# Performance work log

Hardware: AMD Instinct MI355X
Metric: run time of the kernel (lower is better)

## Reference

```python
import jax, jax.numpy as jnp
import numpy as np

N, IN_F, OUT_F, EMB = 8192, 256, 128, 16

def setup_inputs() -> dict:
    key = jax.random.key(0)
    ks = jax.random.split(key, 6)
    s_in, s_out = 1.0 / np.sqrt(IN_F), 1.0 / np.sqrt(OUT_F)
    return {
        "h": jax.random.normal(ks[0], (N, IN_F), jnp.float32),
        "eps": jax.random.normal(ks[1], (N, OUT_F), jnp.float32),
        "a_str": jax.random.uniform(ks[2], (N, N), jnp.float32),  # precomputed exp_adj kernel (positive)
        "W_fc": jax.random.normal(ks[3], (IN_F, OUT_F), jnp.float32) * s_in,
        "W_k": jax.random.normal(ks[4], (OUT_F, EMB), jnp.float32) * s_out,
        "W_q": jax.random.normal(ks[5], (OUT_F, EMB), jnp.float32) * s_out,
    }

def reference(h, eps, a_str, W_fc, W_k, W_q):
    # h0 = fc(h); h <- N(0,1) sample (eps) + h0
    hh = eps + h @ W_fc                      # [N, OUT_F]
    k = hh @ W_k                             # [N, EMB]
    q = hh @ W_q                             # [N, EMB]
    a_att = jax.nn.softmax(k @ q.T, axis=-1) # [N, N]
    a = a_str * a_att                        # elementwise structural mask
    a = a / jnp.sum(a, axis=-1, keepdims=True)  # renormalize rows
    return a @ hh                            # [N, OUT_F]
```

## Files before the change

### kernel.cpp

```cpp
#include <hip/hip_runtime.h>
#include <hip/hip_bf16.h>

#define NN     8192
#define INF_   256
#define OF     128
#define EMBD   16
#define QB     16
#define JB     128
#define NST    (NN / JB)
#define JSPLIT 4
#define NSTP   (NST / JSPLIT)

typedef __attribute__((ext_vector_type(4))) float f32x4;
typedef __attribute__((ext_vector_type(8))) short s16x8;

__device__ __forceinline__ unsigned short f2bf(float x) {
  unsigned u = __builtin_bit_cast(unsigned, x);
  return (unsigned short)((u + 0x7FFFu + ((u >> 16) & 1u)) >> 16);
}

__device__ __forceinline__ float fexp2(float x) {
#if __has_builtin(__builtin_amdgcn_exp2f)
  return __builtin_amdgcn_exp2f(x);
#else
  return exp2f(x);
#endif
}

__global__ __launch_bounds__(256) void k_hh(const float* __restrict__ h,
                                            const float* __restrict__ eps,
                                            const float* __restrict__ Wfc,
                                            float* __restrict__ hh) {
  const int tx = threadIdx.x & 31;
  const int ty = threadIdx.x >> 5;
  const int i0 = blockIdx.x * 16 + ty * 2;
  const int c  = tx * 4;
  f32x4 a0 = *(const f32x4*)&eps[(size_t)i0 * OF + c];
  f32x4 a1 = *(const f32x4*)&eps[(size_t)(i0 + 1) * OF + c];
  const float* h0 = h + (size_t)i0 * INF_;
  const float* h1 = h0 + INF_;
#pragma unroll 2
  for (int kk = 0; kk < INF_; kk += 4) {
    const f32x4 ha = *(const f32x4*)&h0[kk];
    const f32x4 hb = *(const f32x4*)&h1[kk];
#pragma unroll
    for (int u = 0; u < 4; ++u) {
      const f32x4 wv = *(const f32x4*)&Wfc[(size_t)(kk + u) * OF + c];
      a0 += ha[u] * wv;
      a1 += hb[u] * wv;
    }
  }
  *(f32x4*)&hh[(size_t)i0 * OF + c]       = a0;
  *(f32x4*)&hh[(size_t)(i0 + 1) * OF + c] = a1;
}

__global__ __launch_bounds__(256) void k_kq(const float* __restrict__ hh,
                                            const float* __restrict__ Wk,
                                            const float* __restrict__ Wq,
                                            float* __restrict__ kp,
                                            float* __restrict__ qp) {
  const int t   = blockIdx.x * 256 + threadIdx.x;
  const int i   = t >> 3;
  const int sub = t & 7;
  const float* W = (sub < 4) ? Wk : Wq;
  const int e    = (sub & 3) * 4;
  const float* hr = hh + (size_t)i * OF;
  f32x4 acc = {0.f, 0.f, 0.f, 0.f};
#pragma unroll 4
  for (int o = 0; o < OF; o += 4) {
    const f32x4 hv = *(const f32x4*)&hr[o];
#pragma unroll
    for (int u = 0; u < 4; ++u) {
      const f32x4 wv = *(const f32x4*)&W[(size_t)(o + u) * EMBD + e];
      acc += hv[u] * wv;
    }
  }
  if (sub < 4) {
    acc *= 1.4426950408889634f;
    *(f32x4*)&kp[(size_t)i * EMBD + e] = acc;
  } else {
    *(f32x4*)&qp[(size_t)i * EMBD + e] = acc;
  }
}

__global__ __launch_bounds__(256) void k_tr(const float* __restrict__ hh,
                                            short* __restrict__ hhT) {
  __shared__ float tile[64][65];
  const int i0 = blockIdx.x * 64;
  const int o0 = blockIdx.y * 64;
  const int c = threadIdx.x & 63;
  const int r = threadIdx.x >> 6;
#pragma unroll
  for (int rr = 0; rr < 16; ++rr) {
    const int ii = rr * 4 + r;
    tile[ii][c] = hh[(size_t)(i0 + ii) * OF + o0 + c];
  }
  __syncthreads();
#pragma unroll
  for (int rr = 0; rr < 16; ++rr) {
    const int oo = rr * 4 + r;
    hhT[(size_t)(o0 + oo) * NN + i0 + c] = (short)f2bf(tile[c][oo]);
  }
}

__global__ __launch_bounds__(256) void k_attn(const float* __restrict__ Astr,
                                              const float* __restrict__ kp,
                                              const float* __restrict__ qp,
                                              const short* __restrict__ hhT,
                                              float* __restrict__ accP,
                                              float* __restrict__ dP) {
  __shared__ __align__(16) float qbuf[2][JB * EMBD];
  __shared__ __align__(16) short wbuf[2][QB * JB];

  const int tid = threadIdx.x;
  const int l   = tid & 63;
  const int row = tid >> 4;
  const int g   = tid & 15;
  const int ctp = tid >> 6;
  const int h4  = l >> 4;
  const int ln  = l & 15;
  const int rb  = blockIdx.x * QB;
  const int p   = blockIdx.y;
  const int t0  = p * NSTP;
  const int jr  = tid >> 1;
  const int eh  = (tid & 1) * 2;

  float kreg[16];
  {
    const f32x4* kv = (const f32x4*)(kp + (size_t)(rb + row) * EMBD);
#pragma unroll
    for (int i = 0; i < 4; ++i) {
      f32x4 v = kv[i];
      kreg[i * 4 + 0] = v.x; kreg[i * 4 + 1] = v.y;
      kreg[i * 4 + 2] = v.z; kreg[i * 4 + 3] = v.w;
    }
  }
  f32x4 acc0 = {0.f, 0.f, 0.f, 0.f};
  f32x4 acc1 = {0.f, 0.f, 0.f, 0.f};
  float dpart = 0.f;

  const size_t arow = (size_t)(rb + row) * NN;
  const int swzw = row & 7;
  const int qsw0 = (jr >> 3) & 7;

  {
    const float* src = qp + (size_t)(t0 * JB + jr) * EMBD + eh * 4;
    f32x4 v0 = *(const f32x4*)src;
    f32x4 v1 = *(const f32x4*)(src + 4);
    *(f32x4*)&qbuf[0][((jr * 4 + eh)     ^ qsw0) * 4] = v0;
    *(f32x4*)&qbuf[0][((jr * 4 + eh + 1) ^ qsw0) * 4] = v1;
  }
  f32x4 aA[2], aB[2];
  aA[0] = *(const f32x4*)(Astr + arow + t0 * JB + g * 8);
  aA[1] = *(const f32x4*)(Astr + arow + t0 * JB + g * 8 + 4);
  __syncthreads();

  auto STEP = [&](int t, f32x4 (&acur)[2], f32x4 (&anxt)[2], int par) {
    const int jb = t * JB;
    const int tn = (t + 1 < t0 + NSTP) ? (t + 1) : t0;
    const int jn = tn * JB;
    const float* qsrc = qp + (size_t)(jn + jr) * EMBD + eh * 4;
    f32x4 qv0 = *(const f32x4*)qsrc;
    f32x4 qv1 = *(const f32x4*)(qsrc + 4);
    s16x8 bfr[2][4];
#pragma unroll
    for (int cc = 0; cc < 2; ++cc) {
      const size_t bbase = (size_t)(ctp * 32 + cc * 16 + ln) * NN + jb + h4 * 8;
#pragma unroll
      for (int kt = 0; kt < 4; ++kt)
        bfr[cc][kt] = *(const s16x8*)(hhT + bbase + kt * 32);
    }
    anxt[0] = *(const f32x4*)(Astr + arow + jn + g * 8);
    anxt[1] = *(const f32x4*)(Astr + arow + jn + g * 8 + 4);
    float s[8];
#pragma unroll
    for (int jj = 0; jj < 8; ++jj) {
      const int j  = g * 8 + jj;
      const int sw = (j >> 3) & 7;
      const f32x4 q0 = *(const f32x4*)&qbuf[par][((j * 4 + 0) ^ sw) * 4];
      const f32x4 q1 = *(const f32x4*)&qbuf[par][((j * 4 + 1) ^ sw) * 4];
      const f32x4 q2 = *(const f32x4*)&qbuf[par][((j * 4 + 2) ^ sw) * 4];
      const f32x4 q3 = *(const f32x4*)&qbuf[par][((j * 4 + 3) ^ sw) * 4];
      float u0 = kreg[0] * q0.x, u1 = kreg[1] * q0.y;
      u0 = fmaf(kreg[2],  q0.z, u0); u1 = fmaf(kreg[3],  q0.w, u1);
      u0 = fmaf(kreg[4],  q1.x, u0); u1 = fmaf(kreg[5],  q1.y, u1);
      u0 = fmaf(kreg[6],  q1.z, u0); u1 = fmaf(kreg[7],  q1.w, u1);
      u0 = fmaf(kreg[8],  q2.x, u0); u1 = fmaf(kreg[9],  q2.y, u1);
      u0 = fmaf(kreg[10], q2.z, u0); u1 = fmaf(kreg[11], q2.w, u1);
      u0 = fmaf(kreg[12], q3.x, u0); u1 = fmaf(kreg[13], q3.y, u1);
      u0 = fmaf(kreg[14], q3.z, u0); u1 = fmaf(kreg[15], q3.w, u1);
      s[jj] = u0 + u1;
    }
    s16x8 wpack;
    {
      const float* ac = (const float*)&acur[0];
#pragma unroll
      for (int jj = 0; jj < 8; ++jj) {
        const float wv = ac[jj] * fexp2(fminf(s[jj] - 32.0f, 80.0f));
        dpart += wv;
        wpack[jj] = (short)f2bf(wv);
      }
    }
    *(s16x8*)&wbuf[par][row * JB + ((g ^ swzw) * 8)] = wpack;
    *(f32x4*)&qbuf[par ^ 1][((jr * 4 + eh)     ^ qsw0) * 4] = qv0;
    *(f32x4*)&qbuf[par ^ 1][((jr * 4 + eh + 1) ^ qsw0) * 4] = qv1;
    __syncthreads();
    s16x8 afr[4];
#pragma unroll
    for (int kt = 0; kt < 4; ++kt)
      afr[kt] = *(const s16x8*)&wbuf[par][ln * JB + (((kt * 4 + h4) ^ (ln & 7)) * 8)];
#pragma unroll
    for (int kt = 0; kt < 4; ++kt) {
      acc0 = __builtin_amdgcn_mfma_f32_16x16x32_bf16(afr[kt], bfr[0][kt], acc0, 0, 0, 0);
      acc1 = __builtin_amdgcn_mfma_f32_16x16x32_bf16(afr[kt], bfr[1][kt], acc1, 0, 0, 0);
    }
  };

  for (int t = t0; t < t0 + NSTP; t += 2) {
    STEP(t,     aA, aB, 0);
    STEP(t + 1, aB, aA, 1);
  }

  float d = dpart;
  d += __shfl_xor(d, 1, 16);
  d += __shfl_xor(d, 2, 16);
  d += __shfl_xor(d, 4, 16);
  d += __shfl_xor(d, 8, 16);
  if (g == 0) dP[(size_t)p * NN + rb + row] = d;
#pragma unroll
  for (int r = 0; r < 4; ++r) {
    const int lrow = h4 * 4 + r;
    float* orow = accP + ((size_t)p * NN + rb + lrow) * OF + ctp * 32 + ln;
    orow[0]  = acc0[r];
    orow[16] = acc1[r];
  }
}

__global__ __launch_bounds__(256) void k_comb(const float* __restrict__ accP,
                                              const float* __restrict__ dP,
                                              float* __restrict__ out) {
  const int idx = blockIdx.x * 256 + threadIdx.x;
  const int row = idx >> 5;
  const int cq  = (idx & 31) * 4;
  float D = 0.f;
  f32x4 s = {0.f, 0.f, 0.f, 0.f};
#pragma unroll
  for (int pp = 0; pp < JSPLIT; ++pp) {
    D += dP[(size_t)pp * NN + row];
    s += *(const f32x4*)&accP[((size_t)pp * NN + row) * OF + cq];
  }
  const float inv = 1.0f / D;
  f32x4 r = s * inv;
  *(f32x4*)&out[(size_t)row * OF + cq] = r;
}

extern "C" void kernel_launch(void* const* d_in, const int* in_sizes, int n_in,
                              void* d_out, int out_size, void* d_ws, size_t ws_size,
                              hipStream_t stream) {
  const float* h   = (const float*)d_in[0];
  const float* eps = (const float*)d_in[1];
  const float* As  = (const float*)d_in[2];
  const float* Wfc = (const float*)d_in[3];
  const float* Wk  = (const float*)d_in[4];
  const float* Wq  = (const float*)d_in[5];
  float* out = (float*)d_out;

  char* ws = (char*)d_ws;
  float* kp   = (float*)(ws);
  float* qp   = (float*)(ws + (512u << 10));
  short* hhT  = (short*)(ws + (1u << 20));
  float* accP = (float*)(ws + (3u << 20));
  float* hh   = (float*)(ws + (3u << 20));
  float* dP   = (float*)(ws + (19u << 20));

  k_hh<<<NN / 16, 256, 0, stream>>>(h, eps, Wfc, hh);
  k_kq<<<(NN * 8) / 256, 256, 0, stream>>>(hh, Wk, Wq, kp, qp);
  k_tr<<<dim3(NN / 64, OF / 64), 256, 0, stream>>>(hh, hhT);
  k_attn<<<dim3(NN / QB, JSPLIT), 256, 0, stream>>>(As, kp, qp, hhT, accP, dP);
  k_comb<<<(NN * OF / 4) / 256, 256, 0, stream>>>(accP, dP, out);
}
```

Before: 500.3 us.

## Compute attention scores with split-bf16 MFMA and per-wave 32-row tiles

The score computation k·q, previously done with scalar FMAs over q staged in shared memory, now runs on 32x32x16 bf16 MFMAs using a hi/lo bf16 split of k and q (three MFMAs) to keep near-fp32 accuracy. Each wave independently handles 32 query rows over an 8-way j-split, with no shared memory or block barriers, and feeds the bf16 weights straight into register MFMA operands via a row permutation. This removes LDS traffic and syncs and the VALU-bound score math. In exchange it uses more registers and more accP partial storage (8 splits), and drops the exponent clamp.

```diff
diff --git a/kernel.cpp b/kernel.cpp
--- a/kernel.cpp
+++ b/kernel.cpp
@@ -5,20 +5,24 @@
 #define INF_   256
 #define OF     128
 #define EMBD   16
-#define QB     16
-#define JB     128
-#define NST    (NN / JB)
-#define JSPLIT 4
-#define NSTP   (NST / JSPLIT)
-
-typedef __attribute__((ext_vector_type(4))) float f32x4;
-typedef __attribute__((ext_vector_type(8))) short s16x8;
+#define JSPLIT 8
+#define JCH    (NN / JSPLIT)
+#define KV     32
+#define NSTEP  (JCH / KV)
+
+typedef __attribute__((ext_vector_type(4)))  float          f32x4;
+typedef __attribute__((ext_vector_type(16))) float          f32x16;
+typedef __attribute__((ext_vector_type(8)))  short          s16x8;
+typedef __attribute__((ext_vector_type(4)))  unsigned int   u32x4;
+typedef __attribute__((ext_vector_type(4)))  unsigned short u16x4;
 
 __device__ __forceinline__ unsigned short f2bf(float x) {
   unsigned u = __builtin_bit_cast(unsigned, x);
   return (unsigned short)((u + 0x7FFFu + ((u >> 16) & 1u)) >> 16);
 }
-
+__device__ __forceinline__ float bf2f(unsigned short h) {
+  return __builtin_bit_cast(float, (unsigned)h << 16);
+}
 __device__ __forceinline__ float fexp2(float x) {
 #if __has_builtin(__builtin_amdgcn_exp2f)
   return __builtin_amdgcn_exp2f(x);
@@ -57,8 +61,10 @@
 __global__ __launch_bounds__(256) void k_kq(const float* __restrict__ hh,
                                             const float* __restrict__ Wk,
                                             const float* __restrict__ Wq,
-                                            float* __restrict__ kp,
-                                            float* __restrict__ qp) {
+                                            unsigned short* __restrict__ kph,
+                                            unsigned short* __restrict__ kpl,
+                                            unsigned short* __restrict__ qph,
+                                            unsigned short* __restrict__ qpl) {
   const int t   = blockIdx.x * 256 + threadIdx.x;
   const int i   = t >> 3;
   const int sub = t & 7;
@@ -75,12 +81,18 @@
       acc += hv[u] * wv;
     }
   }
-  if (sub < 4) {
-    acc *= 1.4426950408889634f;
-    *(f32x4*)&kp[(size_t)i * EMBD + e] = acc;
-  } else {
-    *(f32x4*)&qp[(size_t)i * EMBD + e] = acc;
-  }
+  if (sub < 4) acc *= 1.4426950408889634f;
+  u16x4 hi4, lo4;
+#pragma unroll
+  for (int u = 0; u < 4; ++u) {
+    const unsigned short hb = f2bf(acc[u]);
+    hi4[u] = hb;
+    lo4[u] = f2bf(acc[u] - bf2f(hb));
+  }
+  unsigned short* dh = (sub < 4) ? kph : qph;
+  unsigned short* dl = (sub < 4) ? kpl : qpl;
+  *(u16x4*)&dh[(size_t)i * EMBD + e] = hi4;
+  *(u16x4*)&dl[(size_t)i * EMBD + e] = lo4;
 }
 
 __global__ __launch_bounds__(256) void k_tr(const float* __restrict__ hh,
@@ -103,136 +115,108 @@
   }
 }
 
-__global__ __launch_bounds__(256) void k_attn(const float* __restrict__ Astr,
-                                              const float* __restrict__ kp,
-                                              const float* __restrict__ qp,
-                                              const short* __restrict__ hhT,
-                                              float* __restrict__ accP,
-                                              float* __restrict__ dP) {
-  __shared__ __align__(16) float qbuf[2][JB * EMBD];
-  __shared__ __align__(16) short wbuf[2][QB * JB];
-
+__global__ __launch_bounds__(256, 2) void k_attn(
+    const float* __restrict__ Astr,
+    const unsigned short* __restrict__ kph,
+    const unsigned short* __restrict__ kpl,
+    const unsigned short* __restrict__ qph,
+    const unsigned short* __restrict__ qpl,
+    const short* __restrict__ hhT,
+    float* __restrict__ accP,
+    float* __restrict__ dP) {
   const int tid = threadIdx.x;
   const int l   = tid & 63;
-  const int row = tid >> 4;
-  const int g   = tid & 15;
-  const int ctp = tid >> 6;
-  const int h4  = l >> 4;
-  const int ln  = l & 15;
-  const int rb  = blockIdx.x * QB;
-  const int p   = blockIdx.y;
-  const int t0  = p * NSTP;
-  const int jr  = tid >> 1;
-  const int eh  = (tid & 1) * 2;
-
-  float kreg[16];
-  {
-    const f32x4* kv = (const f32x4*)(kp + (size_t)(rb + row) * EMBD);
-#pragma unroll
-    for (int i = 0; i < 4; ++i) {
-      f32x4 v = kv[i];
-      kreg[i * 4 + 0] = v.x; kreg[i * 4 + 1] = v.y;
-      kreg[i * 4 + 2] = v.z; kreg[i * 4 + 3] = v.w;
-    }
-  }
-  f32x4 acc0 = {0.f, 0.f, 0.f, 0.f};
-  f32x4 acc1 = {0.f, 0.f, 0.f, 0.f};
+  const int hi  = l >> 5;
+  const int m   = l & 31;
+  const int wid = blockIdx.x * 4 + (tid >> 6);
+  const int p   = wid >> 8;
+  const int qr  = (wid & 255) * 32;
+  const int j0  = p * JCH;
+  const int jperm = (m & 19) | ((m & 8) >> 1) | ((m & 4) << 1);
+
+  const s16x8 kh = *(const s16x8*)(kph + (size_t)(qr + m) * EMBD + hi * 8);
+  const s16x8 kl = *(const s16x8*)(kpl + (size_t)(qr + m) * EMBD + hi * 8);
+
+  const float* ap          = Astr + (size_t)(qr + m) * NN + j0 + hi * 8;
+  const unsigned short* qhb = qph + (size_t)(j0 + jperm) * EMBD + hi * 8;
+  const unsigned short* qlb = qpl + (size_t)(j0 + jperm) * EMBD + hi * 8;
+  const short* hp0 = hhT + (size_t)m * NN + j0 + hi * 8;
+  const short* hp1 = hp0 + (size_t)32 * NN;
+  const short* hp2 = hp0 + (size_t)64 * NN;
+  const short* hp3 = hp0 + (size_t)96 * NN;
+
+  f32x16 acc0 = {}, acc1 = {}, acc2 = {}, acc3 = {};
   float dpart = 0.f;
 
-  const size_t arow = (size_t)(rb + row) * NN;
-  const int swzw = row & 7;
-  const int qsw0 = (jr >> 3) & 7;
-
-  {
-    const float* src = qp + (size_t)(t0 * JB + jr) * EMBD + eh * 4;
-    f32x4 v0 = *(const f32x4*)src;
-    f32x4 v1 = *(const f32x4*)(src + 4);
-    *(f32x4*)&qbuf[0][((jr * 4 + eh)     ^ qsw0) * 4] = v0;
-    *(f32x4*)&qbuf[0][((jr * 4 + eh + 1) ^ qsw0) * 4] = v1;
-  }
-  f32x4 aA[2], aB[2];
-  aA[0] = *(const f32x4*)(Astr + arow + t0 * JB + g * 8);
-  aA[1] = *(const f32x4*)(Astr + arow + t0 * JB + g * 8 + 4);
-  __syncthreads();
-
-  auto STEP = [&](int t, f32x4 (&acur)[2], f32x4 (&anxt)[2], int par) {
-    const int jb = t * JB;
-    const int tn = (t + 1 < t0 + NSTP) ? (t + 1) : t0;
-    const int jn = tn * JB;
-    const float* qsrc = qp + (size_t)(jn + jr) * EMBD + eh * 4;
-    f32x4 qv0 = *(const f32x4*)qsrc;
-    f32x4 qv1 = *(const f32x4*)(qsrc + 4);
-    s16x8 bfr[2][4];
-#pragma unroll
-    for (int cc = 0; cc < 2; ++cc) {
-      const size_t bbase = (size_t)(ctp * 32 + cc * 16 + ln) * NN + jb + h4 * 8;
-#pragma unroll
-      for (int kt = 0; kt < 4; ++kt)
-        bfr[cc][kt] = *(const s16x8*)(hhT + bbase + kt * 32);
-    }
-    anxt[0] = *(const f32x4*)(Astr + arow + jn + g * 8);
-    anxt[1] = *(const f32x4*)(Astr + arow + jn + g * 8 + 4);
-    float s[8];
-#pragma unroll
-    for (int jj = 0; jj < 8; ++jj) {
-      const int j  = g * 8 + jj;
-      const int sw = (j >> 3) & 7;
-      const f32x4 q0 = *(const f32x4*)&qbuf[par][((j * 4 + 0) ^ sw) * 4];
-      const f32x4 q1 = *(const f32x4*)&qbuf[par][((j * 4 + 1) ^ sw) * 4];
-      const f32x4 q2 = *(const f32x4*)&qbuf[par][((j * 4 + 2) ^ sw) * 4];
-      const f32x4 q3 = *(const f32x4*)&qbuf[par][((j * 4 + 3) ^ sw) * 4];
-      float u0 = kreg[0] * q0.x, u1 = kreg[1] * q0.y;
-      u0 = fmaf(kreg[2],  q0.z, u0); u1 = fmaf(kreg[3],  q0.w, u1);
-      u0 = fmaf(kreg[4],  q1.x, u0); u1 = fmaf(kreg[5],  q1.y, u1);
-      u0 = fmaf(kreg[6],  q1.z, u0); u1 = fmaf(kreg[7],  q1.w, u1);
-      u0 = fmaf(kreg[8],  q2.x, u0); u1 = fmaf(kreg[9],  q2.y, u1);
-      u0 = fmaf(kreg[10], q2.z, u0); u1 = fmaf(kreg[11], q2.w, u1);
-      u0 = fmaf(kreg[12], q3.x, u0); u1 = fmaf(kreg[13], q3.y, u1);
-      u0 = fmaf(kreg[14], q3.z, u0); u1 = fmaf(kreg[15], q3.w, u1);
-      s[jj] = u0 + u1;
-    }
-    s16x8 wpack;
-    {
-      const float* ac = (const float*)&acur[0];
-#pragma unroll
-      for (int jj = 0; jj < 8; ++jj) {
-        const float wv = ac[jj] * fexp2(fminf(s[jj] - 32.0f, 80.0f));
-        dpart += wv;
-        wpack[jj] = (short)f2bf(wv);
-      }
-    }
-    *(s16x8*)&wbuf[par][row * JB + ((g ^ swzw) * 8)] = wpack;
-    *(f32x4*)&qbuf[par ^ 1][((jr * 4 + eh)     ^ qsw0) * 4] = qv0;
-    *(f32x4*)&qbuf[par ^ 1][((jr * 4 + eh + 1) ^ qsw0) * 4] = qv1;
-    __syncthreads();
-    s16x8 afr[4];
-#pragma unroll
-    for (int kt = 0; kt < 4; ++kt)
-      afr[kt] = *(const s16x8*)&wbuf[par][ln * JB + (((kt * 4 + h4) ^ (ln & 7)) * 8)];
-#pragma unroll
-    for (int kt = 0; kt < 4; ++kt) {
-      acc0 = __builtin_amdgcn_mfma_f32_16x16x32_bf16(afr[kt], bfr[0][kt], acc0, 0, 0, 0);
-      acc1 = __builtin_amdgcn_mfma_f32_16x16x32_bf16(afr[kt], bfr[1][kt], acc1, 0, 0, 0);
-    }
+  f32x4 aA[4], aB[4];
+  aA[0] = *(const f32x4*)(ap + 0);  aA[1] = *(const f32x4*)(ap + 4);
+  aA[2] = *(const f32x4*)(ap + 16); aA[3] = *(const f32x4*)(ap + 20);
+  aB[0] = *(const f32x4*)(ap + 32); aB[1] = *(const f32x4*)(ap + 36);
+  aB[2] = *(const f32x4*)(ap + 48); aB[3] = *(const f32x4*)(ap + 52);
+
+  auto STEP = [&](int rel, f32x4 (&ac)[4], int rel2) {
+    const size_t qo = (size_t)rel * EMBD;
+    const s16x8 qh = *(const s16x8*)(qhb + qo);
+    const s16x8 ql = *(const s16x8*)(qlb + qo);
+    const s16x8 B00 = *(const s16x8*)(hp0 + rel);
+    const s16x8 B01 = *(const s16x8*)(hp0 + rel + 16);
+    const s16x8 B10 = *(const s16x8*)(hp1 + rel);
+    const s16x8 B11 = *(const s16x8*)(hp1 + rel + 16);
+    const s16x8 B20 = *(const s16x8*)(hp2 + rel);
+    const s16x8 B21 = *(const s16x8*)(hp2 + rel + 16);
+    const s16x8 B30 = *(const s16x8*)(hp3 + rel);
+    const s16x8 B31 = *(const s16x8*)(hp3 + rel + 16);
+    f32x16 sc = {};
+    sc = __builtin_amdgcn_mfma_f32_32x32x16_bf16(qh, kh, sc, 0, 0, 0);
+    sc = __builtin_amdgcn_mfma_f32_32x32x16_bf16(qh, kl, sc, 0, 0, 0);
+    sc = __builtin_amdgcn_mfma_f32_32x32x16_bf16(ql, kh, sc, 0, 0, 0);
+    float w[16];
+    float d0 = 0.f, d1 = 0.f, d2 = 0.f, d3 = 0.f;
+#pragma unroll
+    for (int r = 0; r < 16; ++r) {
+      const float wv = ac[r >> 2][r & 3] * fexp2(sc[r] - 32.0f);
+      w[r] = wv;
+      if ((r & 3) == 0) d0 += wv; else if ((r & 3) == 1) d1 += wv;
+      else if ((r & 3) == 2) d2 += wv; else d3 += wv;
+    }
+    dpart += (d0 + d1) + (d2 + d3);
+    unsigned int pk[8];
+#pragma unroll
+    for (int d = 0; d < 8; ++d) {
+      pk[d] = (unsigned int)f2bf(w[2 * d]) |
+              ((unsigned int)f2bf(w[2 * d + 1]) << 16);
+    }
+    const float* app = ap + rel2;
+    ac[0] = *(const f32x4*)(app);      ac[1] = *(const f32x4*)(app + 4);
+    ac[2] = *(const f32x4*)(app + 16); ac[3] = *(const f32x4*)(app + 20);
+    const s16x8 A1 = __builtin_bit_cast(s16x8, (u32x4){pk[0], pk[1], pk[2], pk[3]});
+    const s16x8 A2 = __builtin_bit_cast(s16x8, (u32x4){pk[4], pk[5], pk[6], pk[7]});
+    acc0 = __builtin_amdgcn_mfma_f32_32x32x16_bf16(A1, B00, acc0, 0, 0, 0);
+    acc0 = __builtin_amdgcn_mfma_f32_32x32x16_bf16(A2, B01, acc0, 0, 0, 0);
+    acc1 = __builtin_amdgcn_mfma_f32_32x32x16_bf16(A1, B10, acc1, 0, 0, 0);
+    acc1 = __builtin_amdgcn_mfma_f32_32x32x16_bf16(A2, B11, acc1, 0, 0, 0);
+    acc2 = __builtin_amdgcn_mfma_f32_32x32x16_bf16(A1, B20, acc2, 0, 0, 0);
+    acc2 = __builtin_amdgcn_mfma_f32_32x32x16_bf16(A2, B21, acc2, 0, 0, 0);
+    acc3 = __builtin_amdgcn_mfma_f32_32x32x16_bf16(A1, B30, acc3, 0, 0, 0);
+    acc3 = __builtin_amdgcn_mfma_f32_32x32x16_bf16(A2, B31, acc3, 0, 0, 0);
   };
 
-  for (int t = t0; t < t0 + NSTP; t += 2) {
-    STEP(t,     aA, aB, 0);
-    STEP(t + 1, aB, aA, 1);
-  }
-
-  float d = dpart;
-  d += __shfl_xor(d, 1, 16);
-  d += __shfl_xor(d, 2, 16);
-  d += __shfl_xor(d, 4, 16);
-  d += __shfl_xor(d, 8, 16);
-  if (g == 0) dP[(size_t)p * NN + rb + row] = d;
-#pragma unroll
-  for (int r = 0; r < 4; ++r) {
-    const int lrow = h4 * 4 + r;
-    float* orow = accP + ((size_t)p * NN + rb + lrow) * OF + ctp * 32 + ln;
-    orow[0]  = acc0[r];
-    orow[16] = acc1[r];
+  for (int tt = 0; tt < NSTEP; tt += 2) {
+    STEP(tt * KV,       aA, ((tt + 2) & (NSTEP - 1)) * KV);
+    STEP((tt + 1) * KV, aB, ((tt + 3) & (NSTEP - 1)) * KV);
+  }
+
+  float dd = dpart + __shfl_xor(dpart, 32);
+  if (hi == 0) dP[(size_t)p * NN + qr + m] = dd;
+
+#pragma unroll
+  for (int r = 0; r < 16; ++r) {
+    const int row = (r & 3) + 8 * (r >> 2) + 4 * hi;
+    float* o = accP + ((size_t)p * NN + qr + row) * OF + m;
+    o[0]  = acc0[r];
+    o[32] = acc1[r];
+    o[64] = acc2[r];
+    o[96] = acc3[r];
   }
 }
 
@@ -249,9 +233,7 @@
     D += dP[(size_t)pp * NN + row];
     s += *(const f32x4*)&accP[((size_t)pp * NN + row) * OF + cq];
   }
-  const float inv = 1.0f / D;
-  f32x4 r = s * inv;
-  *(f32x4*)&out[(size_t)row * OF + cq] = r;
+  *(f32x4*)&out[(size_t)row * OF + cq] = s * (1.0f / D);
 }
 
 extern "C" void kernel_launch(void* const* d_in, const int* in_sizes, int n_in,
@@ -266,16 +248,18 @@
   float* out = (float*)d_out;
 
   char* ws = (char*)d_ws;
-  float* kp   = (float*)(ws);
-  float* qp   = (float*)(ws + (512u << 10));
+  unsigned short* kph = (unsigned short*)(ws);
+  unsigned short* kpl = (unsigned short*)(ws + (256u << 10));
+  unsigned short* qph = (unsigned short*)(ws + (512u << 10));
+  unsigned short* qpl = (unsigned short*)(ws + (768u << 10));
   short* hhT  = (short*)(ws + (1u << 20));
+  float* hh   = (float*)(ws + (3u << 20));
   float* accP = (float*)(ws + (3u << 20));
-  float* hh   = (float*)(ws + (3u << 20));
-  float* dP   = (float*)(ws + (19u << 20));
+  float* dP   = (float*)(ws + (35u << 20));
 
   k_hh<<<NN / 16, 256, 0, stream>>>(h, eps, Wfc, hh);
-  k_kq<<<(NN * 8) / 256, 256, 0, stream>>>(hh, Wk, Wq, kp, qp);
+  k_kq<<<(NN * 8) / 256, 256, 0, stream>>>(hh, Wk, Wq, kph, kpl, qph, qpl);
   k_tr<<<dim3(NN / 64, OF / 64), 256, 0, stream>>>(hh, hhT);
-  k_attn<<<dim3(NN / QB, JSPLIT), 256, 0, stream>>>(As, kp, qp, hhT, accP, dP);
+  k_attn<<<(NN / 32) * JSPLIT / 4, 256, 0, stream>>>(As, kph, kpl, qph, qpl, hhT, accP, dP);
   k_comb<<<(NN * OF / 4) / 256, 256, 0, stream>>>(accP, dP, out);
 }
```

New measurement: 497.7 us. Within noise of the previous version (-0.5%).
